# Performance work log

Hardware: AMD Instinct MI355X
Metric: run time of the kernel (lower is better)

## Reference

```python
import jax, jax.numpy as jnp
import numpy as np

B, L, D, F, K, M = 32, 1024, 384, 384, 3, 4096
LN_EPS = 1e-5


def setup_inputs() -> dict:
    key = jax.random.key(0)
    ks = jax.random.split(key, 6)
    w = lambda k, shp: jax.random.normal(k, shp, jnp.float32) * 0.02
    return {
        "x": jax.random.normal(ks[0], (B, L, D), jnp.float32),
        "target": jax.random.randint(ks[1], (B, L), 0, 5),
        "mel_max_length": M,
        "conv1_w": w(ks[2], (F, D, K)),  # OIW layout
        "conv1_b": jnp.zeros((F,), jnp.float32),
        "ln1_g": jnp.ones((F,), jnp.float32),
        "ln1_b": jnp.zeros((F,), jnp.float32),
        "conv2_w": w(ks[3], (F, F, K)),
        "conv2_b": jnp.zeros((F,), jnp.float32),
        "ln2_g": jnp.ones((F,), jnp.float32),
        "ln2_b": jnp.zeros((F,), jnp.float32),
        "lin_w": w(ks[4], (F, 1)),
        "lin_b": jnp.zeros((1,), jnp.float32),
    }


def conv1d_same(x, w, b):
    # x: [B, L, C], w: [O, I, K] -> [B, L, O], 'same' padding
    pad = (w.shape[-1] - 1) // 2
    y = jax.lax.conv_general_dilated(
        x, w, window_strides=(1,), padding=[(pad, pad)],
        dimension_numbers=("NWC", "OIW", "NWC"))
    return y + b


def layernorm(x, g, b):
    m = jnp.mean(x, axis=-1, keepdims=True)
    v = jnp.mean(jnp.square(x - m), axis=-1, keepdims=True)
    return (x - m) * jax.lax.rsqrt(v + LN_EPS) * g + b


def duration_predictor(x, c1w, c1b, g1, b1, c2w, c2b, g2, b2, lw, lb):
    h = jnp.maximum(layernorm(conv1d_same(x, c1w, c1b), g1, b1), 0.0)
    h = jnp.maximum(layernorm(conv1d_same(h, c2w, c2b), g2, b2), 0.0)
    return jnp.maximum(h @ lw + lb, 0.0)[..., 0]  # [B, L]


def length_regulate(x, durations, mel_max_length):
    # Equivalent to one-hot alignment matmul + zero pad, done as a gather.
    cum = jnp.cumsum(durations, axis=1)  # [B, L]
    t = jnp.arange(mel_max_length)       # [M]
    # frame t belongs to phoneme j where cum[j-1] <= t < cum[j]
    idx = jax.vmap(lambda c: jnp.searchsorted(c, t, side="right"))(cum)  # [B, M]
    valid = (t[None, :] < cum[:, -1:]).astype(x.dtype)                    # [B, M]
    idx = jnp.minimum(idx, durations.shape[1] - 1)
    out = jnp.take_along_axis(x, idx[..., None], axis=1) * valid[..., None]
    return out  # [B, M, D]


def reference(x, target, mel_max_length, conv1_w, conv1_b, ln1_g, ln1_b,
              conv2_w, conv2_b, ln2_g, ln2_b, lin_w, lin_b):
    dur_pred = duration_predictor(x, conv1_w, conv1_b, ln1_g, ln1_b,
                                  conv2_w, conv2_b, ln2_g, ln2_b, lin_w, lin_b)
    out = length_regulate(x, target, mel_max_length)
    return out, dur_pred
```

## Files before the change

kernel.cpp:

```cpp
#include <hip/hip_runtime.h>

#define DEV __device__ __forceinline__

typedef unsigned short u16;
typedef __attribute__((ext_vector_type(8))) short bf16x8;
typedef __attribute__((ext_vector_type(8))) unsigned short u16x8;
typedef __attribute__((ext_vector_type(4))) float f32x4;

constexpr int Bz = 32, Lz = 1024, Dz = 384, Fz = 384, KWz = 3, Mz = 4096;
constexpr float EPS = 1e-5f;

DEV u16 f2bf(float f) {
  unsigned u = __float_as_uint(f);
  u += 0x7fffu + ((u >> 16) & 1u);
  return (u16)(u >> 16);
}

typedef __attribute__((address_space(1))) const unsigned char ga_t;
typedef __attribute__((address_space(3))) unsigned char la_t;
DEV void gload16(const void* g, void* l) {
  __builtin_amdgcn_global_load_lds((ga_t*)g, (la_t*)l, 16, 0, 0);
}

#define WAITV(n) asm volatile("s_waitcnt vmcnt(" #n ")" ::: "memory")

__global__ __launch_bounds__(1024) void k_pre(
    const float* __restrict__ w1, const float* __restrict__ w2,
    u16* __restrict__ w1t, u16* __restrict__ w2t, u16* __restrict__ h1,
    const int* __restrict__ tgt, int* __restrict__ idxb) {
  __shared__ int sc[Lz];
  constexpr int WT = KWz * Fz * Dz;
  constexpr int PREP_ELEMS = 2 * WT + Bz * 2 * Dz;
  constexpr int PREP_BLKS = (PREP_ELEMS + 1023) / 1024;
  const int tid = threadIdx.x;

  if (blockIdx.x < PREP_BLKS) {
    int gid = blockIdx.x * 1024 + tid;
    if (gid < WT) {
      int k = gid / (Fz * Dz), rem = gid % (Fz * Dz);
      int f = rem / Dz, d = rem % Dz;
      w1t[gid] = f2bf(w1[(f * Dz + d) * KWz + k]);
    } else if (gid < 2 * WT) {
      int g2 = gid - WT;
      int k = g2 / (Fz * Fz), rem = g2 % (Fz * Fz);
      int co = rem / Fz, ci = rem % Fz;
      w2t[g2] = f2bf(w2[(co * Fz + ci) * KWz + k]);
    } else if (gid < PREP_ELEMS) {
      int p = gid - 2 * WT;
      int b = p / (2 * Dz), r = (p / Dz) & 1, d = p % Dz;
      size_t row = (size_t)b * (Lz + 2) + (r ? (Lz + 1) : 0);
      h1[row * Dz + d] = 0;
    }
    return;
  }
  int b = blockIdx.x - PREP_BLKS;
  sc[tid] = tgt[b * Lz + tid];
  __syncthreads();
  for (int off = 1; off < Lz; off <<= 1) {
    int add = (tid >= off) ? sc[tid - off] : 0;
    __syncthreads();
    sc[tid] += add;
    __syncthreads();
  }
  int total = sc[Lz - 1];
  for (int t = tid; t < Mz; t += 1024) {
    int lo = 0, hi = Lz;
    while (lo < hi) {
      int mid = (lo + hi) >> 1;
      if (sc[mid] > t) hi = mid; else lo = mid + 1;
    }
    int iv = (t < total) ? (lo > Lz - 1 ? Lz - 1 : lo) : -1;
    idxb[b * Mz + t] = iv;
  }
}

__global__ void k_gather(const float* __restrict__ x, const int* __restrict__ idxb,
                         float* __restrict__ out) {
  int wid = (blockIdx.x * blockDim.x + threadIdx.x) >> 6;
  int lane = threadIdx.x & 63;
  int nw = (gridDim.x * blockDim.x) >> 6;
  for (int row = wid; row < Bz * Mz; row += nw) {
    int b = row >> 12;
    int iv = idxb[row];
    float4* dst = reinterpret_cast<float4*>(out + (size_t)row * Dz);
    if (iv < 0) {
      float4 z = make_float4(0.f, 0.f, 0.f, 0.f);
      dst[lane] = z;
      if (lane < 32) dst[64 + lane] = z;
    } else {
      const float4* src =
          reinterpret_cast<const float4*>(x + ((size_t)b * Lz + iv) * Dz);
      dst[lane] = src[lane];
      if (lane < 32) dst[64 + lane] = src[64 + lane];
    }
  }
}

template <int LAYER>
__global__ __launch_bounds__(512, 2) void k_conv(
    const void* __restrict__ Asrc,
    const u16* __restrict__ wt,
    const float* __restrict__ cbias,
    const float* __restrict__ lng, const float* __restrict__ lnb,
    u16* __restrict__ hout,
    const float* __restrict__ lw, const float* __restrict__ lbias,
    float* __restrict__ dur)
{
  constexpr int ABUFS = (LAYER == 1) ? 2 : 3;
  __shared__ __align__(16) u16 Ash[ABUFS][8192];
  __shared__ __align__(16) u16 Bsh[3][384 * 32];
  __shared__ float s_sum[4][128], s_sq[4][128], s_dot[4][128];

  const int tid = threadIdx.x;
  const int lane = tid & 63, wave = tid >> 6;
  const int wr = wave >> 2, wc = wave & 3;
  const int l15 = lane & 15, lh = lane >> 4;
  const int b = blockIdx.x >> 3, l0 = (blockIdx.x & 7) << 7;
  const bf16x8 zfrag = {0, 0, 0, 0, 0, 0, 0, 0};

  int bgof[3], bldo[3];
  #pragma unroll
  for (int i = 0; i < 3; ++i) {
    int c = wave + 8 * i;
    int slot = c * 64 + lane, f = slot >> 2, q = slot & 3;
    int ks = q ^ ((f >> 1) & 3);
    bgof[i] = f * 384 + ks * 8;
    bldo[i] = c * 512;
  }
  auto STAGE_B = [&](int kt) {
    int tap = kt % 3, dw = kt / 3;
    const u16* sb = wt + tap * (384 * 384) + dw * 32;
    u16* dst = Bsh[tap];
    #pragma unroll
    for (int i = 0; i < 3; ++i) gload16(sb + bgof[i], dst + bldo[i]);
  };

  const float* arow_ptr = nullptr;
  const u16* a2src[2] = {nullptr, nullptr};
  int a2ldo[2] = {0, 0};
  float4 ar0, ar1, ar2, ar3;
  if constexpr (LAYER == 1) {
    int r1 = tid & 255, g1 = tid >> 8;
    int grow = l0 - 1 + r1;
    if (grow > l0 + 135) grow = l0 + 135;
    if (grow < 0) grow = 0;
    if (grow > Lz - 1) grow = Lz - 1;
    arow_ptr = (const float*)Asrc + (size_t)b * Lz * 384 + (size_t)grow * 384 +
               g1 * 8;
  } else {
    #pragma unroll
    for (int i = 0; i < 2; ++i) {
      int c = wave + 8 * i;
      int s = c * 64 + lane, g = s >> 8, r = s & 255;
      int p = l0 + r;
      if (p > l0 + 135) p = l0 + 135;
      if (p > Lz + 1) p = Lz + 1;
      a2src[i] = (const u16*)Asrc + (size_t)b * (Lz + 2) * 384 +
                 (size_t)p * 384 + g * 8;
      a2ldo[i] = c * 512;
    }
  }
  auto AISSUE = [&](int w) {
    const float* p = arow_ptr + w * 32;
    ar0 = *reinterpret_cast<const float4*>(p);
    ar1 = *reinterpret_cast<const float4*>(p + 4);
    ar2 = *reinterpret_cast<const float4*>(p + 16);
    ar3 = *reinterpret_cast<const float4*>(p + 20);
  };
  auto ADSW = [&](int wbuf) {
    u16x8 h0, h1;
    h0[0] = f2bf(ar0.x); h0[1] = f2bf(ar0.y); h0[2] = f2bf(ar0.z); h0[3] = f2bf(ar0.w);
    h0[4] = f2bf(ar1.x); h0[5] = f2bf(ar1.y); h0[6] = f2bf(ar1.z); h0[7] = f2bf(ar1.w);
    h1[0] = f2bf(ar2.x); h1[1] = f2bf(ar2.y); h1[2] = f2bf(ar2.z); h1[3] = f2bf(ar2.w);
    h1[4] = f2bf(ar3.x); h1[5] = f2bf(ar3.y); h1[6] = f2bf(ar3.z); h1[7] = f2bf(ar3.w);
    *reinterpret_cast<u16x8*>(&Ash[wbuf][tid * 8]) = h0;
    *reinterpret_cast<u16x8*>(&Ash[wbuf][(tid + 512) * 8]) = h1;
  };
  auto STAGE_A2 = [&](int w, int buf) {
    #pragma unroll
    for (int i = 0; i < 2; ++i) gload16(a2src[i] + w * 32, &Ash[buf][a2ldo[i]]);
  };

  int tr[4], boff[6];
  #pragma unroll
  for (int m = 0; m < 4; ++m) tr[m] = wr * 64 + m * 16 + l15;
  #pragma unroll
  for (int n = 0; n < 6; ++n) {
    int c = wc * 96 + n * 16 + l15;
    boff[n] = c * 32 + (lh ^ ((c >> 1) & 3)) * 8;
  }

  f32x4 acc[4][6] = {};

  if constexpr (LAYER == 1) {
    AISSUE(0);
    WAITV(0);
    ADSW(0);
    AISSUE(1);
    __builtin_amdgcn_sched_barrier(0);
    STAGE_B(0);
    STAGE_B(1);
  } else {
    STAGE_A2(0, 0);
    STAGE_B(0);
    STAGE_A2(1, 1);
    STAGE_B(1);
  }

#define PHASE(T)                                                               \
  {                                                                            \
    if constexpr ((T) == 0) {                                                  \
      if constexpr (LAYER == 2) {                                              \
        if (w == 0) { WAITV(5); } else { WAITV(3); }                           \
      } else { WAITV(3); }                                                     \
    } else if constexpr ((T) == 1) {                                           \
      if (w <= 9) {                                                            \
        if constexpr (LAYER == 1) { WAITV(7); } else { WAITV(5); }             \
      } else { WAITV(3); }                                                     \
    } else {                                                                   \
      if (w <= 9) {                                                            \
        if constexpr (LAYER == 1) { WAITV(7); } else { WAITV(5); }             \
      } else if (w == 10) { WAITV(3); } else { WAITV(0); }                     \
    }                                                                          \
    asm volatile("s_waitcnt lgkmcnt(0)" ::: "memory");                         \
    __builtin_amdgcn_s_barrier();                                              \
    __builtin_amdgcn_sched_barrier(0);                                         \
    if constexpr (LAYER == 1 && (T) == 0) {                                    \
      if (w <= 10) ADSW((w + 1) & 1);                                          \
    }                                                                          \
    const int abuf_ = (LAYER == 1) ? (w & 1) : (w % 3);                        \
    bf16x8 av[4], bv[6];                                                       \
    _Pragma("unroll")                                                          \
    for (int m = 0; m < 4; ++m) {                                              \
      av[m] = *reinterpret_cast<const bf16x8*>(                                \
          &Ash[abuf_][(lh * 256 + tr[m] + (T)) * 8]);                          \
      if constexpr (LAYER == 1 && (T) != 1) {                                  \
        int gr = l0 + tr[m] + (T) - 1;                                         \
        if ((unsigned)gr > (unsigned)(Lz - 1)) av[m] = zfrag;                  \
      }                                                                        \
    }                                                                          \
    _Pragma("unroll")                                                          \
    for (int n = 0; n < 6; ++n)                                                \
      bv[n] = *reinterpret_cast<const bf16x8*>(&Bsh[(T)][boff[n]]);            \
    __builtin_amdgcn_sched_barrier(0);                                         \
    { int kt2_ = 3 * w + (T) + 2; if (kt2_ <= 35) STAGE_B(kt2_); }             \
    __builtin_amdgcn_sched_barrier(0);                                         \
    if constexpr ((T) == 0) {                                                  \
      if (w <= 9) {                                                            \
        if constexpr (LAYER == 1) { AISSUE(w + 2); }                           \
        else { STAGE_A2(w + 2, (w + 2) % 3); }                                 \
      }                                                                        \
    }                                                                          \
    __builtin_amdgcn_sched_barrier(0);                                         \
    _Pragma("unroll")                                                          \
    for (int m = 0; m < 4; ++m)                                                \
      _Pragma("unroll")                                                        \
      for (int n = 0; n < 6; ++n)                                              \
        acc[m][n] = __builtin_amdgcn_mfma_f32_16x16x32_bf16(av[m], bv[n],      \
                                                            acc[m][n], 0, 0, 0);\
  }

  for (int w = 0; w < 12; ++w) {
    PHASE(0)
    PHASE(1)
    PHASE(2)
  }
#undef PHASE

  __syncthreads();
  float gv[6], bvv[6], cbv[6], lwv[6];
  #pragma unroll
  for (int n = 0; n < 6; ++n) {
    int c = wc * 96 + n * 16 + l15;
    gv[n] = lng[c]; bvv[n] = lnb[c]; cbv[n] = cbias[c];
    lwv[n] = (LAYER == 2) ? lw[c] : 0.f;
  }
  #pragma unroll
  for (int m = 0; m < 4; ++m) {
    #pragma unroll
    for (int r = 0; r < 4; ++r) {
      float s = 0.f, q2 = 0.f;
      #pragma unroll
      for (int n = 0; n < 6; ++n) {
        float v = acc[m][n][r] + cbv[n];
        s += v; q2 += v * v;
      }
      #pragma unroll
      for (int off = 1; off < 16; off <<= 1) {
        s += __shfl_xor(s, off);
        q2 += __shfl_xor(q2, off);
      }
      if (l15 == 0) {
        int row = wr * 64 + m * 16 + lh * 4 + r;
        s_sum[wc][row] = s;
        s_sq[wc][row] = q2;
      }
    }
  }
  __syncthreads();
  #pragma unroll
  for (int m = 0; m < 4; ++m) {
    #pragma unroll
    for (int r = 0; r < 4; ++r) {
      int row = wr * 64 + m * 16 + lh * 4 + r;
      float S = 0.f, Q = 0.f;
      #pragma unroll
      for (int w = 0; w < 4; ++w) { S += s_sum[w][row]; Q += s_sq[w][row]; }
      float mean = S * (1.f / 384.f);
      float var = Q * (1.f / 384.f) - mean * mean;
      float rstd = rsqrtf(var + EPS);
      float dotp = 0.f;
      #pragma unroll
      for (int n = 0; n < 6; ++n) {
        float v = acc[m][n][r] + cbv[n];
        float y = fmaxf((v - mean) * rstd * gv[n] + bvv[n], 0.f);
        if constexpr (LAYER == 1) {
          int c = wc * 96 + n * 16 + l15;
          hout[((size_t)(b * (Lz + 2) + l0 + row + 1)) * 384 + c] = f2bf(y);
        } else {
          dotp += y * lwv[n];
        }
      }
      if constexpr (LAYER == 2) {
        #pragma unroll
        for (int off = 1; off < 16; off <<= 1) dotp += __shfl_xor(dotp, off);
        if (l15 == 0) s_dot[wc][row] = dotp;
      }
    }
  }
  if constexpr (LAYER == 2) {
    __syncthreads();
    if (tid < 128) {
      float dsum = lbias[0];
      #pragma unroll
      for (int w = 0; w < 4; ++w) dsum += s_dot[w][tid];
      dur[(size_t)b * Lz + l0 + tid] = fmaxf(dsum, 0.f);
    }
  }
}

extern "C" void kernel_launch(void* const* d_in, const int* in_sizes, int n_in,
                              void* d_out, int out_size, void* d_ws, size_t ws_size,
                              hipStream_t stream) {
  (void)in_sizes; (void)n_in; (void)out_size; (void)ws_size;
  const float* x   = (const float*)d_in[0];
  const int* tgt   = (const int*)d_in[1];
  const float* w1  = (const float*)d_in[3];
  const float* c1b = (const float*)d_in[4];
  const float* g1  = (const float*)d_in[5];
  const float* b1  = (const float*)d_in[6];
  const float* w2  = (const float*)d_in[7];
  const float* c2b = (const float*)d_in[8];
  const float* g2  = (const float*)d_in[9];
  const float* b2  = (const float*)d_in[10];
  const float* lw  = (const float*)d_in[11];
  const float* lb  = (const float*)d_in[12];

  float* out0 = (float*)d_out;
  float* dur  = out0 + (size_t)Bz * Mz * Dz;

  const size_t h1_n = (size_t)Bz * (Lz + 2) * Dz;
  const size_t wt_n = (size_t)KWz * Fz * Dz;
  u16* h1  = (u16*)d_ws;
  u16* w1t = h1 + h1_n;
  u16* w2t = w1t + wt_n;
  int* idxb = (int*)(w2t + wt_n);

  constexpr int PREP_BLKS =
      (2 * KWz * Fz * Dz + Bz * 2 * Dz + 1023) / 1024;
  k_pre<<<PREP_BLKS + Bz, 1024, 0, stream>>>(w1, w2, w1t, w2t, h1, tgt, idxb);
  k_conv<1><<<256, 512, 0, stream>>>(x, w1t, c1b, g1, b1, h1, nullptr, nullptr,
                                     nullptr);
  k_conv<2><<<256, 512, 0, stream>>>(h1, w2t, c2b, g2, b2, nullptr, lw, lb, dur);
  k_gather<<<2048, 256, 0, stream>>>(x, idxb, out0);
}
```

Baseline: 122.5 us.

## Load conv weight fragments directly into registers, dropping LDS staging of B

Conv weight (B operand) tiles are no longer staged through shared memory via global_load_lds. Each wave now loads its bf16x8 weight fragments straight from global memory into double-buffered registers, prefetching the next tap's fragments while the current MFMAs run. Barriers drop from one per tap to one per 32-wide K chunk, and LDS use shrinks, which could raise occupancy. The trade is redundant global/L2 traffic, since waves sharing columns each fetch the same weights, plus uncoalesced 16-byte row-strided loads and more register pressure. The single fixed vmcnt wait may also under- or over-synchronize against the mixed A and B loads.

Measured after the change: 188.2 us. 1.54x slower.

```diff
diff --git a/kernel.cpp b/kernel.cpp
--- a/kernel.cpp
+++ b/kernel.cpp
@@ -108,7 +108,6 @@
 {
   constexpr int ABUFS = (LAYER == 1) ? 2 : 3;
   __shared__ __align__(16) u16 Ash[ABUFS][8192];
-  __shared__ __align__(16) u16 Bsh[3][384 * 32];
   __shared__ float s_sum[4][128], s_sq[4][128], s_dot[4][128];
 
   const int tid = threadIdx.x;
@@ -118,22 +117,13 @@
   const int b = blockIdx.x >> 3, l0 = (blockIdx.x & 7) << 7;
   const bf16x8 zfrag = {0, 0, 0, 0, 0, 0, 0, 0};
 
-  int bgof[3], bldo[3];
-  #pragma unroll
-  for (int i = 0; i < 3; ++i) {
-    int c = wave + 8 * i;
-    int slot = c * 64 + lane, f = slot >> 2, q = slot & 3;
-    int ks = q ^ ((f >> 1) & 3);
-    bgof[i] = f * 384 + ks * 8;
-    bldo[i] = c * 512;
-  }
-  auto STAGE_B = [&](int kt) {
-    int tap = kt % 3, dw = kt / 3;
-    const u16* sb = wt + tap * (384 * 384) + dw * 32;
-    u16* dst = Bsh[tap];
-    #pragma unroll
-    for (int i = 0; i < 3; ++i) gload16(sb + bgof[i], dst + bldo[i]);
-  };
+  int pboff[6];
+  #pragma unroll
+  for (int n = 0; n < 6; ++n) {
+    int c = wc * 96 + n * 16 + l15;
+    pboff[n] = c * 384 + lh * 8;
+  }
+  bf16x8 pB0[6], pB1[6];
 
   const float* arow_ptr = nullptr;
   const u16* a2src[2] = {nullptr, nullptr};
@@ -181,14 +171,9 @@
     for (int i = 0; i < 2; ++i) gload16(a2src[i] + w * 32, &Ash[buf][a2ldo[i]]);
   };
 
-  int tr[4], boff[6];
+  int tr[4];
   #pragma unroll
   for (int m = 0; m < 4; ++m) tr[m] = wr * 64 + m * 16 + l15;
-  #pragma unroll
-  for (int n = 0; n < 6; ++n) {
-    int c = wc * 96 + n * 16 + l15;
-    boff[n] = c * 32 + (lh ^ ((c >> 1) & 3)) * 8;
-  }
 
   f32x4 acc[4][6] = {};
 
@@ -197,39 +182,36 @@
     WAITV(0);
     ADSW(0);
     AISSUE(1);
-    __builtin_amdgcn_sched_barrier(0);
-    STAGE_B(0);
-    STAGE_B(1);
   } else {
     STAGE_A2(0, 0);
-    STAGE_B(0);
     STAGE_A2(1, 1);
-    STAGE_B(1);
-  }
-
-#define PHASE(T)                                                               \
+  }
+  __builtin_amdgcn_sched_barrier(0);
+  #pragma unroll
+  for (int n = 0; n < 6; ++n)
+    pB0[n] = *reinterpret_cast<const bf16x8*>(wt + pboff[n]);
+
+#define BLOAD(T_, W_, PBV)                                                     \
+  {                                                                            \
+    const u16* src_ = wt + (T_) * (384 * 384) + (W_) * 32;                     \
+    _Pragma("unroll")                                                          \
+    for (int n = 0; n < 6; ++n)                                                \
+      PBV[n] = *reinterpret_cast<const bf16x8*>(src_ + pboff[n]);              \
+  }
+
+#define PHASE(W, T, PBU, PBV)                                                  \
   {                                                                            \
     if constexpr ((T) == 0) {                                                  \
-      if constexpr (LAYER == 2) {                                              \
-        if (w == 0) { WAITV(5); } else { WAITV(3); }                           \
-      } else { WAITV(3); }                                                     \
-    } else if constexpr ((T) == 1) {                                           \
-      if (w <= 9) {                                                            \
-        if constexpr (LAYER == 1) { WAITV(7); } else { WAITV(5); }             \
-      } else { WAITV(3); }                                                     \
-    } else {                                                                   \
-      if (w <= 9) {                                                            \
-        if constexpr (LAYER == 1) { WAITV(7); } else { WAITV(5); }             \
-      } else if (w == 10) { WAITV(3); } else { WAITV(0); }                     \
+      WAITV(6);                \
+      asm volatile("s_waitcnt lgkmcnt(0)" ::: "memory");                       \
+      __builtin_amdgcn_s_barrier();                                            \
+      __builtin_amdgcn_sched_barrier(0);                                       \
+      if constexpr (LAYER == 1) {                                              \
+        if ((W) <= 10) ADSW(((W) + 1) & 1);                                    \
+      }                                                                        \
     }                                                                          \
-    asm volatile("s_waitcnt lgkmcnt(0)" ::: "memory");                         \
-    __builtin_amdgcn_s_barrier();                                              \
-    __builtin_amdgcn_sched_barrier(0);                                         \
-    if constexpr (LAYER == 1 && (T) == 0) {                                    \
-      if (w <= 10) ADSW((w + 1) & 1);                                          \
-    }                                                                          \
-    const int abuf_ = (LAYER == 1) ? (w & 1) : (w % 3);                        \
-    bf16x8 av[4], bv[6];                                                       \
+    const int abuf_ = (LAYER == 1) ? ((W) & 1) : ((W) % 3);                    \
+    bf16x8 av[4];                                                              \
     _Pragma("unroll")                                                          \
     for (int m = 0; m < 4; ++m) {                                              \
       av[m] = *reinterpret_cast<const bf16x8*>(                                \
@@ -239,33 +221,35 @@
         if ((unsigned)gr > (unsigned)(Lz - 1)) av[m] = zfrag;                  \
       }                                                                        \
     }                                                                          \
-    _Pragma("unroll")                                                          \
-    for (int n = 0; n < 6; ++n)                                                \
-      bv[n] = *reinterpret_cast<const bf16x8*>(&Bsh[(T)][boff[n]]);            \
-    __builtin_amdgcn_sched_barrier(0);                                         \
-    { int kt2_ = 3 * w + (T) + 2; if (kt2_ <= 35) STAGE_B(kt2_); }             \
-    __builtin_amdgcn_sched_barrier(0);                                         \
+                                             \
+    if constexpr ((T) < 2) { BLOAD((T) + 1, (W), PBV); }                       \
+    else if ((W) < 11)     { BLOAD(0, (W) + 1, PBV); }                         \
     if constexpr ((T) == 0) {                                                  \
-      if (w <= 9) {                                                            \
-        if constexpr (LAYER == 1) { AISSUE(w + 2); }                           \
-        else { STAGE_A2(w + 2, (w + 2) % 3); }                                 \
+      if ((W) <= 9) {                                                          \
+        if constexpr (LAYER == 1) { AISSUE((W) + 2); }                         \
+        else { STAGE_A2((W) + 2, ((W) + 2) % 3); }                             \
       }                                                                        \
     }                                                                          \
-    __builtin_amdgcn_sched_barrier(0);                                         \
     _Pragma("unroll")                                                          \
     for (int m = 0; m < 4; ++m)                                                \
       _Pragma("unroll")                                                        \
       for (int n = 0; n < 6; ++n)                                              \
-        acc[m][n] = __builtin_amdgcn_mfma_f32_16x16x32_bf16(av[m], bv[n],      \
+        acc[m][n] = __builtin_amdgcn_mfma_f32_16x16x32_bf16(av[m], PBU[n],     \
                                                             acc[m][n], 0, 0, 0);\
   }
 
-  for (int w = 0; w < 12; ++w) {
-    PHASE(0)
-    PHASE(1)
-    PHASE(2)
+  for (int w2 = 0; w2 < 6; ++w2) {
+    const int we = 2 * w2;
+    PHASE(we, 0, pB0, pB1)
+    PHASE(we, 1, pB1, pB0)
+    PHASE(we, 2, pB0, pB1)
+    const int wo = 2 * w2 + 1;
+    PHASE(wo, 0, pB1, pB0)
+    PHASE(wo, 1, pB0, pB1)
+    PHASE(wo, 2, pB1, pB0)
   }
 #undef PHASE
+#undef BLOAD
 
   __syncthreads();
   float gv[6], bvv[6], cbv[6], lwv[6];
```
